# Performance work log

Hardware: AMD Instinct MI355X
Metric: run time of the kernel (lower is better)

## Reference

```python
import jax, jax.numpy as jnp
import numpy as np


def conv2d(x, w, groups=1, pad=0):
    # x: [N,C,H,W], w: [O, C//groups, kh, kw]
    return jax.lax.conv_general_dilated(
        x, w, window_strides=(1, 1), padding=[(pad, pad), (pad, pad)],
        dimension_numbers=("NCHW", "OIHW", "NCHW"), feature_group_count=groups)


def l2norm(x, eps=1e-12):
    # torch F.normalize over last dim: x / max(||x||_2, eps)
    n = jnp.sqrt(jnp.sum(x * x, axis=-1, keepdims=True))
    return x / jnp.maximum(n, eps)


def setup_inputs() -> dict:
    key = jax.random.key(0)
    dim, heads, b, H, W = 48, 8, 2, 256, 256
    ks = jax.random.split(key, 20)
    rn = lambda k, shp, s: (jax.random.normal(k, shp, dtype=jnp.float32) * s)
    return {
        "x1": rn(ks[0], (b, dim, H, W), 1.0),
        "x2": rn(ks[1], (b, dim, H, W), 1.0),
        "t1": jnp.ones((heads, 1, 1), jnp.float32),
        "t2": jnp.ones((heads, 1, 1), jnp.float32),
        "qkv1_w": rn(ks[2], (dim * 3, dim, 1, 1), 0.05),
        "qkv1_dw": rn(ks[3], (dim * 3, 1, 3, 3), 0.05),
        "qkv2_w": rn(ks[4], (dim * 3, dim, 1, 1), 0.05),
        "qkv2_dw": rn(ks[5], (dim * 3, 1, 3, 3), 0.05),
        "mid1_w": rn(ks[6], (dim, dim, 1, 1), 0.05),
        "mid2_w": rn(ks[7], (dim, dim, 1, 1), 0.05),
        "pE_w": rn(ks[8], (dim * 8, dim * 2, 1, 1), 0.05),
        "pE_dw": rn(ks[9], (dim * 8, 1, 3, 3), 0.05),
        "pE1_w": rn(ks[10], (dim * 4, dim, 1, 1), 0.05),
        "pE1_dw": rn(ks[11], (dim * 4, 1, 3, 3), 0.05),
        "pE2_w": rn(ks[12], (dim * 4, dim, 1, 1), 0.05),
        "pE2_dw": rn(ks[13], (dim * 4, 1, 3, 3), 0.05),
        "po1_w": rn(ks[14], (dim * 2, dim * 4, 1, 1), 0.05),
        "po2_w": rn(ks[15], (dim * 2, dim * 4, 1, 1), 0.05),
    }


def reference(x1, x2, t1, t2, qkv1_w, qkv1_dw, qkv2_w, qkv2_dw,
              mid1_w, mid2_w, pE_w, pE_dw, pE1_w, pE1_dw,
              pE2_w, pE2_dw, po1_w, po2_w):
    b, c, h, w = x1.shape
    heads = t1.shape[0]
    ch = c // heads  # channels per head

    def to_heads(t):  # [b, c, h, w] -> [b, heads, ch, h*w]
        return t.reshape(b, heads, ch, h * w)

    qkv1 = conv2d(conv2d(x1, qkv1_w), qkv1_dw, groups=3 * c, pad=1)
    q1, k1, v1 = jnp.split(qkv1, 3, axis=1)
    qkv2 = conv2d(conv2d(x2, qkv2_w), qkv2_dw, groups=3 * c, pad=1)
    q2, k2, v2 = jnp.split(qkv2, 3, axis=1)

    q1, k1, v1 = to_heads(q1), to_heads(k1), to_heads(v1)
    q2, k2, v2 = to_heads(q2), to_heads(k2), to_heads(v2)
    q1, k1 = l2norm(q1), l2norm(k1)
    q2, k2 = l2norm(q2), l2norm(k2)

    # channel cross-attention: [b, heads, ch, ch]
    attn1 = jnp.einsum("bhcn,bhdn->bhcd", q2, k1) * t1
    attn2 = jnp.einsum("bhcn,bhdn->bhcd", q1, k2) * t2
    out1 = jnp.einsum("bhcd,bhdn->bhcn", jax.nn.softmax(attn1, axis=-1), v1)
    out2 = jnp.einsum("bhcd,bhdn->bhcn", jax.nn.softmax(attn2, axis=-1), v2)
    out1 = out1.reshape(b, c, h, w)
    out2 = out2.reshape(b, c, h, w)

    x1 = x1 + conv2d(out1, mid1_w)
    x2 = x2 + conv2d(out2, mid2_w)
    out = jnp.concatenate([x1, x2], axis=1)  # [b, 2c, h, w]

    g = conv2d(conv2d(out, pE_w), pE_dw, groups=8 * c, pad=1)  # [b, 8c, h, w]
    g1, g2 = jnp.split(g, 2, axis=1)
    x1 = jax.nn.gelu(g1, approximate=False) * conv2d(conv2d(x1, pE1_w), pE1_dw, groups=4 * c, pad=1)
    x2 = jax.nn.gelu(g2, approximate=False) * conv2d(conv2d(x2, pE2_w), pE2_dw, groups=4 * c, pad=1)

    return out + conv2d(x1, po1_w) + conv2d(x2, po2_w)
```

## Files before the change

kernel.cpp:

```cpp
#include <hip/hip_runtime.h>
#include <math.h>

#define HW_ 65536

typedef __attribute__((ext_vector_type(8))) short b16x8;
typedef __attribute__((ext_vector_type(4))) short b16x4;
typedef __attribute__((ext_vector_type(4))) float f32x4;

__device__ __forceinline__ unsigned short f2b(float f) {
    union { float f; unsigned u; } v; v.f = f;
    unsigned r = v.u + 0x7fffu + ((v.u >> 16) & 1u);
    return (unsigned short)(r >> 16);
}
__device__ __forceinline__ float b2f(unsigned short h) {
    union { unsigned u; float f; } v; v.u = ((unsigned)h) << 16; return v.f;
}
__device__ __forceinline__ float gelu_f(float x) {
    float t = 0.7978845608f * fmaf(0.044715f * x, x * x, x);
    float e = __expf(2.f * t);
    float th = 1.f - 2.f / (e + 1.f);
    return 0.5f * x * (1.f + th);
}

__device__ __forceinline__ float wave_reduce_sum(float v) {
    #pragma unroll
    for (int off = 32; off; off >>= 1) v += __shfl_down(v, off, 64);
    return v;
}

__device__ __forceinline__ size_t baddr(long px, int CC, int g) {
    return (((size_t)(px >> 4)) * CC + g) * 128 + ((size_t)(px & 15) << 3);
}

__global__ __launch_bounds__(256) void wprep_k(
    const float* __restrict__ q1w, const float* __restrict__ q2w,
    const float* __restrict__ m1w, const float* __restrict__ m2w,
    const float* __restrict__ pEw, const float* __restrict__ p1w,
    const float* __restrict__ p2w, const float* __restrict__ o1w,
    const float* __restrict__ o2w,
    const float* __restrict__ q1dw, const float* __restrict__ q2dw,
    const float* __restrict__ pEdw, const float* __restrict__ p1dw,
    const float* __restrict__ p2dw,
    unsigned short* __restrict__ wt, float* __restrict__ dwt)
{
    const int idx = blockIdx.x * 256 + threadIdx.x;
    if (idx < 135168) {
        const int base[8] = {0,9216,18432,21504,24576,61440,98304,116736};
        int s = 0;
        #pragma unroll
        for (int i = 1; i < 8; i++) if (idx >= base[i]) s = i;
        const int local = idx - base[s];
        float v = 0.f;
        if (s < 4) {
            const int m = local >> 6, k = local & 63;
            const float* src = (s == 0) ? q1w : (s == 1) ? q2w : (s == 2) ? m1w : m2w;
            if (k < 48) v = src[m * 48 + k];
        } else if (s < 6) {
            const int br = s - 4;
            const int m = local / 96, k = local % 96;
            if (m < 192) {
                v = pEw[(size_t)(br * 192 + m) * 96 + k];
            } else {
                const float* p12 = br ? p2w : p1w;
                const int lo = br * 48, m2 = m - 192;
                if (k >= lo && k < lo + 48) v = p12[m2 * 48 + (k - lo)];
            }
        } else {
            const int m = local / 192, k = local % 192;
            v = ((s == 6) ? o1w : o2w)[m * 192 + k];
        }
        wt[idx] = f2b(v);
    } else if (idx < 135168 + 9504) {
        const int d = idx - 135168;
        const int dbase[5] = {0,1296,2592,6048,7776};
        const int Cs[5] = {144,144,384,192,192};
        int s = 0;
        #pragma unroll
        for (int i = 1; i < 5; i++) if (d >= dbase[i]) s = i;
        const int local = d - dbase[s], C = Cs[s];
        const int t = local / C, c = local % C;
        const float* src = (s == 0) ? q1dw : (s == 1) ? q2dw : (s == 2) ? pEdw
                         : (s == 3) ? p1dw : p2dw;
        dwt[d] = src[c * 9 + t];
    }
}

template<int BM, int KC, int NT, int BSRC, int EPI, bool GRIDSWAP>
__global__ __launch_bounds__(256) void gemm_k(
    const unsigned short* __restrict__ B16,
    const float* __restrict__ Bf32, int Cin,
    const unsigned short* __restrict__ W16,
    unsigned short* __restrict__ out16, int CCo, int Coff,
    float* __restrict__ outf, const unsigned short* __restrict__ res)
{
    constexpr int MF = BM / 16;
    const int tid = threadIdx.x;
    const int lane = tid & 63, w = tid >> 6;
    const int lm = lane & 15, lk = lane >> 4;
    const int mb = GRIDSWAP ? blockIdx.x : blockIdx.y;
    const int pxblk = GRIDSWAP ? blockIdx.y : blockIdx.x;
    const int m0 = mb * BM;
    const long wavepx = ((long)pxblk * 4 + w) * (NT * 16);
    const long pxb0 = wavepx >> 4;

    f32x4 acc[NT][MF];
    #pragma unroll
    for (int nt = 0; nt < NT; nt++)
        #pragma unroll
        for (int m = 0; m < MF; m++)
            #pragma unroll
            for (int j = 0; j < 4; j++) acc[nt][m][j] = 0.f;

    #pragma unroll
    for (int kc = 0; kc < KC; kc++) {
        b16x8 a[MF];
        #pragma unroll
        for (int m = 0; m < MF; m++)
            a[m] = *(const b16x8*)&W16[(size_t)(m0 + m * 16 + lm) * (KC * 32) + kc * 32 + lk * 8];
        #pragma unroll
        for (int nt = 0; nt < NT; nt++) {
            b16x8 bb;
            if (BSRC == 0) {
                bb = *(const b16x8*)&B16[((pxb0 + nt) * (KC * 4) + (kc * 4 + lk)) * 128 + lm * 8];
            } else {
                const long px = wavepx + nt * 16 + lm;
                const int p = (int)(px & 65535), bat = (int)(px >> 16);
                #pragma unroll
                for (int j = 0; j < 8; j++) {
                    const int c = kc * 32 + lk * 8 + j;
                    float v = (c < Cin) ? Bf32[((size_t)(bat * Cin + c) << 16) + p] : 0.f;
                    bb[j] = (short)f2b(v);
                }
            }
            #pragma unroll
            for (int m = 0; m < MF; m++)
                acc[nt][m] = __builtin_amdgcn_mfma_f32_16x16x32_bf16(a[m], bb, acc[nt][m], 0, 0, 0);
        }
    }

    #pragma unroll
    for (int nt = 0; nt < NT; nt++) {
        const long px = wavepx + nt * 16 + lm;
        #pragma unroll
        for (int m = 0; m < MF; m++) {
            const int mrow = m * 16 + lk * 4;
            if (EPI == 0) {
                b16x4 o;
                #pragma unroll
                for (int j = 0; j < 4; j++) o[j] = (short)f2b(acc[nt][m][j]);
                const int ch = Coff + m0 + mrow;
                *(b16x4*)&out16[((pxb0 + nt) * CCo + (ch >> 3)) * 128 + lm * 8 + (ch & 7)] = o;
            } else if (EPI == 1) {
                const int p = (int)(px & 65535), bat = (int)(px >> 16);
                b16x4 r4 = *(const b16x4*)&res[((pxb0 + nt) * 12 + (mrow >> 3)) * 128 + lm * 8 + (mrow & 7)];
                #pragma unroll
                for (int j = 0; j < 4; j++)
                    outf[((size_t)(bat * 96 + mrow + j) << 16) + p]
                        = acc[nt][m][j] + b2f((unsigned short)r4[j]);
            } else {
                const int p = (int)(px & 65535), bat = (int)(px >> 16);
                #pragma unroll
                for (int j = 0; j < 4; j++) {
                    const size_t adr = ((size_t)(bat * 96 + mrow + j) << 16) + p;
                    outf[adr] += acc[nt][m][j];
                }
            }
        }
    }
}

__device__ __forceinline__ void dw_acc8(
    float acc[4][8], const unsigned short* __restrict__ T, int CC, int g,
    long px0, int y, int x0, const float* __restrict__ wt, int wstr)
{
    #pragma unroll
    for (int dy = -1; dy <= 1; dy++) {
        const int yy = y + dy;
        if ((unsigned)yy >= 256u) continue;
        float w[3][8];
        #pragma unroll
        for (int t = 0; t < 3; t++) {
            const float* wp = wt + (size_t)((dy + 1) * 3 + t) * wstr;
            const float4 a = *(const float4*)wp;
            const float4 b = *(const float4*)(wp + 4);
            w[t][0] = a.x; w[t][1] = a.y; w[t][2] = a.z; w[t][3] = a.w;
            w[t][4] = b.x; w[t][5] = b.y; w[t][6] = b.z; w[t][7] = b.w;
        }
        #pragma unroll
        for (int c = 0; c < 6; c++) {
            const int xx = x0 - 1 + c;
            b16x8 v;
            if ((unsigned)xx < 256u) {
                v = *(const b16x8*)&T[baddr(px0 + dy * 256 + (c - 1), CC, g)];
            } else {
                #pragma unroll
                for (int k = 0; k < 8; k++) v[k] = 0;
            }
            float f[8];
            #pragma unroll
            for (int k = 0; k < 8; k++) f[k] = b2f((unsigned short)v[k]);
            const int ilo = (c - 2 < 0) ? 0 : c - 2;
            const int ihi = (c < 3) ? c : 3;
            #pragma unroll
            for (int i = ilo; i <= ihi; i++)
                #pragma unroll
                for (int j = 0; j < 8; j++)
                    acc[i][j] = fmaf(w[c - i][j], f[j], acc[i][j]);
        }
    }
}

__global__ __launch_bounds__(256) void dw144_k(
    const unsigned short* __restrict__ in1, unsigned short* __restrict__ out1,
    const unsigned short* __restrict__ in2, unsigned short* __restrict__ out2,
    const float* __restrict__ dwt)
{
    const int z = blockIdx.z;
    const unsigned short* in = z ? in2 : in1;
    unsigned short* out = z ? out2 : out1;
    const float* wt = dwt + z * 1296;
    const int bx = blockIdx.x;
    const int sb = (bx & 7) * 288 + (bx >> 3);
    const int idx = sb * 256 + threadIdx.x;
    const int pb = idx / 72;
    const int rem = idx - pb * 72;
    const int g = rem >> 2, i = rem & 3;
    const long px0 = (long)pb * 16 + i * 4;
    const int y = (int)((px0 & 65535) >> 8), x0 = (int)(px0 & 255);

    float acc[4][8];
    #pragma unroll
    for (int a = 0; a < 4; a++)
        #pragma unroll
        for (int j = 0; j < 8; j++) acc[a][j] = 0.f;
    dw_acc8(acc, in, 18, g, px0, y, x0, wt + g * 8, 144);
    #pragma unroll
    for (int a = 0; a < 4; a++) {
        b16x8 o;
        #pragma unroll
        for (int j = 0; j < 8; j++) o[j] = (short)f2b(acc[a][j]);
        *(b16x8*)&out[baddr(px0 + a, 18, g)] = o;
    }
}

__global__ __launch_bounds__(256) void dwtail_k(
    const unsigned short* __restrict__ GH, unsigned short* __restrict__ Xg,
    const float* __restrict__ dwtG, const float* __restrict__ dwtH)
{
    const int bx = blockIdx.x;
    const int sb = (bx & 7) * 384 + (bx >> 3);
    const int idx = sb * 256 + threadIdx.x;
    const int pb = idx / 96;
    const int rem = idx - pb * 96;
    const int g = rem >> 2, i = rem & 3;
    const long px0 = (long)pb * 16 + i * 4;
    const int y = (int)((px0 & 65535) >> 8), x0 = (int)(px0 & 255);

    float aG[4][8], aH[4][8];
    #pragma unroll
    for (int a = 0; a < 4; a++)
        #pragma unroll
        for (int j = 0; j < 8; j++) { aG[a][j] = 0.f; aH[a][j] = 0.f; }
    dw_acc8(aG, GH, 48, g,      px0, y, x0, dwtG + g * 8, 384);
    dw_acc8(aH, GH, 48, 24 + g, px0, y, x0, dwtH + g * 8, 192);

    #pragma unroll
    for (int a = 0; a < 4; a++) {
        b16x8 o;
        #pragma unroll
        for (int j = 0; j < 8; j++)
            o[j] = (short)f2b(gelu_f(aG[a][j]) * aH[a][j]);
        *(b16x8*)&Xg[baddr(px0 + a, 24, g)] = o;
    }
}

__global__ __launch_bounds__(256) void attnA_k(
    const unsigned short* __restrict__ Q1, const unsigned short* __restrict__ Q2,
    float* __restrict__ part)
{
    const int tid = threadIdx.x;
    const int chunk = blockIdx.x, bh = blockIdx.y, a = blockIdx.z;
    const int b = bh >> 3, h = bh & 7;
    const unsigned* Qq = (const unsigned*)(a ? Q1 : Q2);
    const unsigned* Qk = (const unsigned*)(a ? Q2 : Q1);
    const int u0 = h * 3;
    const int cq = u0 >> 2, o = u0 & 3;
    const int ck = (24 + u0) >> 2;

    float dot[36], nq[6], nk[6];
    #pragma unroll
    for (int i = 0; i < 36; i++) dot[i] = 0.f;
    #pragma unroll
    for (int i = 0; i < 6; i++) { nq[i] = 0.f; nk[i] = 0.f; }

    #pragma unroll 1
    for (int r = 0; r < 8; r++) {
        const long px = (long)b * 65536 + chunk * 2048 + r * 256 + tid;
        const size_t rowu = ((size_t)(px >> 4)) * 18 * 64 + ((px & 15) << 2);
        const uint4 qa = *(const uint4*)&Qq[rowu + (size_t)cq * 64];
        const uint4 qb = *(const uint4*)&Qq[rowu + (size_t)(cq + 1) * 64];
        const uint4 ka = *(const uint4*)&Qk[rowu + (size_t)ck * 64];
        const uint4 kb = *(const uint4*)&Qk[rowu + (size_t)(ck + 1) * 64];
        unsigned uq[3], uk[3];
        if (o == 0)      { uq[0]=qa.x; uq[1]=qa.y; uq[2]=qa.z; uk[0]=ka.x; uk[1]=ka.y; uk[2]=ka.z; }
        else if (o == 1) { uq[0]=qa.y; uq[1]=qa.z; uq[2]=qa.w; uk[0]=ka.y; uk[1]=ka.z; uk[2]=ka.w; }
        else if (o == 2) { uq[0]=qa.z; uq[1]=qa.w; uq[2]=qb.x; uk[0]=ka.z; uk[1]=ka.w; uk[2]=kb.x; }
        else             { uq[0]=qa.w; uq[1]=qb.x; uq[2]=qb.y; uk[0]=ka.w; uk[1]=kb.x; uk[2]=kb.y; }
        float q[6], k[6];
        #pragma unroll
        for (int i = 0; i < 3; i++) {
            union { unsigned u; float f; } lo, hi;
            lo.u = uq[i] << 16; hi.u = uq[i] & 0xFFFF0000u;
            q[2 * i] = lo.f; q[2 * i + 1] = hi.f;
            lo.u = uk[i] << 16; hi.u = uk[i] & 0xFFFF0000u;
            k[2 * i] = lo.f; k[2 * i + 1] = hi.f;
        }
        #pragma unroll
        for (int c = 0; c < 6; c++) nq[c] = fmaf(q[c], q[c], nq[c]);
        #pragma unroll
        for (int d = 0; d < 6; d++) nk[d] = fmaf(k[d], k[d], nk[d]);
        #pragma unroll
        for (int c = 0; c < 6; c++)
            #pragma unroll
            for (int d = 0; d < 6; d++) dot[c * 6 + d] = fmaf(q[c], k[d], dot[c * 6 + d]);
    }

    __shared__ float red[4][48];
    const int lane = tid & 63, wid = tid >> 6;
    #pragma unroll
    for (int i = 0; i < 48; i++) {
        float v = (i < 36) ? dot[i] : (i < 42 ? nq[i - 36] : nk[i - 42]);
        v = wave_reduce_sum(v);
        if (!lane) red[wid][i] = v;
    }
    __syncthreads();
    if (tid < 48)
        part[((size_t)((a * 16 + bh) * 32 + chunk)) * 48 + tid]
            = red[0][tid] + red[1][tid] + red[2][tid] + red[3][tid];
}

__global__ void attnB_k(const float* __restrict__ part,
                        const float* __restrict__ t1, const float* __restrict__ t2,
                        float* __restrict__ att)
{
    const int abh = blockIdx.x, tid = threadIdx.x;
    const int a = abh >> 4, b = (abh >> 3) & 1, h = abh & 7;
    __shared__ float s[48];
    if (tid < 48) {
        float v = 0.f;
        for (int ch = 0; ch < 32; ch++) v += part[((size_t)abh * 32 + ch) * 48 + tid];
        s[tid] = v;
    }
    __syncthreads();
    if (tid < 6) {
        const int c = tid;
        const float tv = a ? t2[h] : t1[h];
        const float qn = fmaxf(sqrtf(s[36 + c]), 1e-12f);
        float raw[6];
        #pragma unroll
        for (int d = 0; d < 6; d++)
            raw[d] = tv * s[c * 6 + d] / (qn * fmaxf(sqrtf(s[42 + d]), 1e-12f));
        float m = raw[0];
        #pragma unroll
        for (int d = 1; d < 6; d++) m = fmaxf(m, raw[d]);
        float e[6], sum = 0.f;
        #pragma unroll
        for (int d = 0; d < 6; d++) { e[d] = expf(raw[d] - m); sum += e[d]; }
        const float inv = 1.f / sum;
        #pragma unroll
        for (int d = 0; d < 6; d++)
            att[((size_t)(a * 2 + b) * 8 + h) * 36 + c * 6 + d] = e[d] * inv;
    }
}

__global__ __launch_bounds__(256) void mid_k(
    const unsigned short* __restrict__ Q1, const unsigned short* __restrict__ Q2,
    const float* __restrict__ att,
    const float* __restrict__ x1, const float* __restrict__ x2,
    const unsigned short* __restrict__ Wm, unsigned short* __restrict__ D16p)
{
    const int br = blockIdx.y;
    const unsigned short* Qv = br ? Q2 : Q1;
    const float* x = br ? x2 : x1;
    const unsigned short* W16 = Wm + br * 3072;
    const float* attb = att + br * 576;
    const int boff = br * 48;

    __shared__ float atts[288];
    __shared__ unsigned short S[256][72];
    const int tid = threadIdx.x;
    const long px = (long)blockIdx.x * 256 + tid;
    const int bat = (int)(px >> 16);

    for (int i = tid; i < 288; i += 256) atts[i] = attb[bat * 288 + i];

    float v[48];
    #pragma unroll
    for (int i = 0; i < 6; i++) {
        b16x8 t = *(const b16x8*)&Qv[baddr(px, 18, 12 + i)];
        #pragma unroll
        for (int j = 0; j < 8; j++) v[i * 8 + j] = b2f((unsigned short)t[j]);
    }
    __syncthreads();

    #pragma unroll
    for (int h = 0; h < 8; h++) {
        unsigned short sh[6];
        #pragma unroll
        for (int c = 0; c < 6; c++) {
            float s = 0.f;
            #pragma unroll
            for (int d = 0; d < 6; d++) s = fmaf(atts[h * 36 + c * 6 + d], v[h * 6 + d], s);
            sh[c] = f2b(s);
        }
        #pragma unroll
        for (int i = 0; i < 3; i++) {
            unsigned packed = (unsigned)sh[2 * i] | ((unsigned)sh[2 * i + 1] << 16);
            *(unsigned*)&S[tid][h * 6 + 2 * i] = packed;
        }
    }
    #pragma unroll
    for (int i = 0; i < 8; i++) *(unsigned*)&S[tid][48 + 2 * i] = 0u;
    __syncthreads();

    const int lane = tid & 63, w = tid >> 6;
    const int lm = lane & 15, lk = lane >> 4;
    f32x4 acc[4][3];
    #pragma unroll
    for (int nt = 0; nt < 4; nt++)
        #pragma unroll
        for (int m = 0; m < 3; m++)
            #pragma unroll
            for (int j = 0; j < 4; j++) acc[nt][m][j] = 0.f;

    #pragma unroll
    for (int kc = 0; kc < 2; kc++) {
        b16x8 a[3];
        #pragma unroll
        for (int m = 0; m < 3; m++)
            a[m] = *(const b16x8*)&W16[(size_t)(m * 16 + lm) * 64 + kc * 32 + lk * 8];
        #pragma unroll
        for (int nt = 0; nt < 4; nt++) {
            b16x8 bb = *(const b16x8*)&S[w * 64 + nt * 16 + lm][kc * 32 + lk * 8];
            #pragma unroll
            for (int m = 0; m < 3; m++)
                acc[nt][m] = __builtin_amdgcn_mfma_f32_16x16x32_bf16(a[m], bb, acc[nt][m], 0, 0, 0);
        }
    }

    #pragma unroll
    for (int nt = 0; nt < 4; nt++) {
        const long px2 = (long)blockIdx.x * 256 + w * 64 + nt * 16 + lm;
        const int p2 = (int)(px2 & 65535);
        const long pxb2 = px2 >> 4;
        #pragma unroll
        for (int m = 0; m < 3; m++) {
            const int row = m * 16 + lk * 4;
            b16x4 o;
            #pragma unroll
            for (int j = 0; j < 4; j++) {
                float xv = x[((size_t)(bat * 48 + row + j) << 16) + p2];
                o[j] = (short)f2b(acc[nt][m][j] + xv);
            }
            const int ch = boff + row;
            *(b16x4*)&D16p[(pxb2 * 12 + (ch >> 3)) * 128 + lm * 8 + (ch & 7)] = o;
        }
    }
}

extern "C" void kernel_launch(void* const* d_in, const int* in_sizes, int n_in,
                              void* d_out, int out_size, void* d_ws, size_t ws_size,
                              hipStream_t stream) {
    const float* x1      = (const float*)d_in[0];
    const float* x2      = (const float*)d_in[1];
    const float* t1      = (const float*)d_in[2];
    const float* t2      = (const float*)d_in[3];
    const float* qkv1_w  = (const float*)d_in[4];
    const float* qkv1_dw = (const float*)d_in[5];
    const float* qkv2_w  = (const float*)d_in[6];
    const float* qkv2_dw = (const float*)d_in[7];
    const float* mid1_w  = (const float*)d_in[8];
    const float* mid2_w  = (const float*)d_in[9];
    const float* pE_w    = (const float*)d_in[10];
    const float* pE_dw   = (const float*)d_in[11];
    const float* pE1_w   = (const float*)d_in[12];
    const float* pE1_dw  = (const float*)d_in[13];
    const float* pE2_w   = (const float*)d_in[14];
    const float* pE2_dw  = (const float*)d_in[15];
    const float* po1_w   = (const float*)d_in[16];
    const float* po2_w   = (const float*)d_in[17];
    float* dout = (float*)d_out;
    char* ws = (char*)d_ws;

    unsigned short* D16p  = (unsigned short*)(ws + 0);
    unsigned short* QKVc1 = (unsigned short*)(ws + 25165824);
    unsigned short* QKVc2 = (unsigned short*)(ws + 62914560);
    unsigned short* Q1    = (unsigned short*)(ws + 100663296);
    unsigned short* Q2    = (unsigned short*)(ws + 138412032);
    unsigned short* GH    = (unsigned short*)(ws + 25165824);
    unsigned short* Xg    = (unsigned short*)(ws + 125829120);
    float*          PART  = (float*)(ws + 176160768);
    float*          ATT   = (float*)(ws + 176357376);
    unsigned short* W16   = (unsigned short*)(ws + 176361984);
    float*          DWT   = (float*)(ws + 176632320);

    const dim3 blk(256);

    wprep_k<<<dim3(566), blk, 0, stream>>>(
        qkv1_w, qkv2_w, mid1_w, mid2_w, pE_w, pE1_w, pE2_w, po1_w, po2_w,
        qkv1_dw, qkv2_dw, pE_dw, pE1_dw, pE2_dw, W16, DWT);

    gemm_k<144,2,4,1,0,false><<<dim3(512,1), blk, 0, stream>>>(
        nullptr, x1, 48, W16, QKVc1, 18, 0, nullptr, nullptr);
    gemm_k<144,2,4,1,0,false><<<dim3(512,1), blk, 0, stream>>>(
        nullptr, x2, 48, W16 + 9216, QKVc2, 18, 0, nullptr, nullptr);
    dw144_k<<<dim3(2304,1,2), blk, 0, stream>>>(QKVc1, Q1, QKVc2, Q2, DWT);

    attnA_k<<<dim3(32,16,2), blk, 0, stream>>>(Q1, Q2, PART);
    attnB_k<<<dim3(32), dim3(64), 0, stream>>>(PART, t1, t2, ATT);

    mid_k<<<dim3(512,2), blk, 0, stream>>>(Q1, Q2, ATT, x1, x2, W16 + 18432, D16p);

    for (int br = 0; br < 2; br++) {
        gemm_k<192,3,2,0,0,true><<<dim3(2,1024), blk, 0, stream>>>(
            D16p, nullptr, 0, W16 + 24576 + br * 36864, GH, 48, 0,
            nullptr, nullptr);
        dwtail_k<<<dim3(3072), blk, 0, stream>>>(
            GH, Xg, DWT + 2592 + br * 192, DWT + (br ? 7776 : 6048));
        if (br == 0)
            gemm_k<96,6,4,0,1,false><<<dim3(512,1), blk, 0, stream>>>(
                Xg, nullptr, 0, W16 + 98304, nullptr, 0, 0, dout, D16p);
        else
            gemm_k<96,6,4,0,2,false><<<dim3(512,1), blk, 0, stream>>>(
                Xg, nullptr, 0, W16 + 116736, nullptr, 0, 0, dout, nullptr);
    }
}
```

Measured before the change: 411.9 us.

## Rewrite depthwise conv row loads with precomputed addresses and retune GEMM tiles

The depthwise 3x3 kernels now compute a base address once and load each row as six 16-byte chunks, using precomputed left/right neighbour offsets instead of calling baddr per tap. bf16 values are unpacked with shifts and masks. The dwtail kernel gets a launch-bounds occupancy hint. Several GEMM launches are retuned to smaller tile counts with twice as many blocks, trading per-block reuse for more parallelism.

```diff
diff --git a/kernel.cpp b/kernel.cpp
--- a/kernel.cpp
+++ b/kernel.cpp
@@ -169,43 +169,50 @@
     }
 }
 
-__device__ __forceinline__ void dw_acc8(
-    float acc[4][8], const unsigned short* __restrict__ T, int CC, int g,
-    long px0, int y, int x0, const float* __restrict__ wt, int wstr)
-{
-    #pragma unroll
-    for (int dy = -1; dy <= 1; dy++) {
-        const int yy = y + dy;
-        if ((unsigned)yy >= 256u) continue;
-        float w[3][8];
-        #pragma unroll
-        for (int t = 0; t < 3; t++) {
-            const float* wp = wt + (size_t)((dy + 1) * 3 + t) * wstr;
-            const float4 a = *(const float4*)wp;
-            const float4 b = *(const float4*)(wp + 4);
-            w[t][0] = a.x; w[t][1] = a.y; w[t][2] = a.z; w[t][3] = a.w;
-            w[t][4] = b.x; w[t][5] = b.y; w[t][6] = b.z; w[t][7] = b.w;
-        }
-        #pragma unroll
-        for (int c = 0; c < 6; c++) {
-            const int xx = x0 - 1 + c;
-            b16x8 v;
-            if ((unsigned)xx < 256u) {
-                v = *(const b16x8*)&T[baddr(px0 + dy * 256 + (c - 1), CC, g)];
-            } else {
-                #pragma unroll
-                for (int k = 0; k < 8; k++) v[k] = 0;
-            }
-            float f[8];
-            #pragma unroll
-            for (int k = 0; k < 8; k++) f[k] = b2f((unsigned short)v[k]);
-            const int ilo = (c - 2 < 0) ? 0 : c - 2;
-            const int ihi = (c < 3) ? c : 3;
-            #pragma unroll
-            for (int i = ilo; i <= ihi; i++)
+__device__ __forceinline__ void unpack8(const uint4 u, float f[8]) {
+    union { unsigned u; float f; } a;
+    a.u = u.x << 16;         f[0] = a.f;
+    a.u = u.x & 0xFFFF0000u; f[1] = a.f;
+    a.u = u.y << 16;         f[2] = a.f;
+    a.u = u.y & 0xFFFF0000u; f[3] = a.f;
+    a.u = u.z << 16;         f[4] = a.f;
+    a.u = u.z & 0xFFFF0000u; f[5] = a.f;
+    a.u = u.w << 16;         f[6] = a.f;
+    a.u = u.w & 0xFFFF0000u; f[7] = a.f;
+}
+
+__device__ __forceinline__ void dw_row4(
+    float acc[4][8], const unsigned short* __restrict__ T,
+    size_t cb, long lOff, long rOff, bool lval, bool rval,
+    const float* __restrict__ wrow, int wstr)
+{
+    float w[3][8];
+    #pragma unroll
+    for (int tx = 0; tx < 3; tx++) {
+        const float4 a = *(const float4*)(wrow + (size_t)tx * wstr);
+        const float4 b = *(const float4*)(wrow + (size_t)tx * wstr + 4);
+        w[tx][0] = a.x; w[tx][1] = a.y; w[tx][2] = a.z; w[tx][3] = a.w;
+        w[tx][4] = b.x; w[tx][5] = b.y; w[tx][6] = b.z; w[tx][7] = b.w;
+    }
+    uint4 u[6];
+    if (lval) u[0] = *(const uint4*)&T[cb + lOff];
+    else      u[0] = make_uint4(0u, 0u, 0u, 0u);
+    #pragma unroll
+    for (int c = 0; c < 4; c++) u[c + 1] = *(const uint4*)&T[cb + (size_t)c * 8];
+    if (rval) u[5] = *(const uint4*)&T[cb + rOff];
+    else      u[5] = make_uint4(0u, 0u, 0u, 0u);
+
+    #pragma unroll
+    for (int d = 0; d < 6; d++) {
+        float f[8];
+        unpack8(u[d], f);
+        #pragma unroll
+        for (int tx = 0; tx < 3; tx++) {
+            const int p = d - tx;
+            if (p >= 0 && p < 4)
                 #pragma unroll
                 for (int j = 0; j < 8; j++)
-                    acc[i][j] = fmaf(w[c - i][j], f[j], acc[i][j]);
+                    acc[p][j] = fmaf(w[tx][j], f[j], acc[p][j]);
         }
     }
 }
@@ -222,55 +229,88 @@
     const int bx = blockIdx.x;
     const int sb = (bx & 7) * 288 + (bx >> 3);
     const int idx = sb * 256 + threadIdx.x;
-    const int pb = idx / 72;
-    const int rem = idx - pb * 72;
+    const int pbi = idx / 72;
+    const int rem = idx - pbi * 72;
     const int g = rem >> 2, i = rem & 3;
-    const long px0 = (long)pb * 16 + i * 4;
-    const int y = (int)((px0 & 65535) >> 8), x0 = (int)(px0 & 255);
+    const long px0 = (long)pbi * 16 + i * 4;
+    const int x0 = (int)(px0 & 255);
+    const int y = (int)((px0 >> 8) & 255);
+    const bool lval = x0 > 0, rval = x0 < 252;
+    const int off = (int)(px0 & 15) * 8;
+    const size_t cb0 = ((size_t)(px0 >> 4) * 18 + g) * 128 + off;
+    const long lOff = (off == 0) ? (120 - 18 * 128) : -8;
+    const long rOff = (off == 96) ? (18 * 128 - 96) : 32;
+    const long dyStep = 16 * 18 * 128;
 
     float acc[4][8];
     #pragma unroll
-    for (int a = 0; a < 4; a++)
-        #pragma unroll
-        for (int j = 0; j < 8; j++) acc[a][j] = 0.f;
-    dw_acc8(acc, in, 18, g, px0, y, x0, wt + g * 8, 144);
-    #pragma unroll
-    for (int a = 0; a < 4; a++) {
+    for (int p = 0; p < 4; p++)
+        #pragma unroll
+        for (int j = 0; j < 8; j++) acc[p][j] = 0.f;
+
+    #pragma unroll
+    for (int dy = -1; dy <= 1; dy++) {
+        const int yy = y + dy;
+        if ((unsigned)yy >= 256u) continue;
+        const size_t cb = cb0 + (size_t)((long)dy * dyStep);
+        dw_row4(acc, in, cb, lOff, rOff, lval, rval,
+                wt + g * 8 + (size_t)(dy + 1) * 3 * 144, 144);
+    }
+
+    #pragma unroll
+    for (int p = 0; p < 4; p++) {
         b16x8 o;
         #pragma unroll
-        for (int j = 0; j < 8; j++) o[j] = (short)f2b(acc[a][j]);
-        *(b16x8*)&out[baddr(px0 + a, 18, g)] = o;
-    }
-}
-
-__global__ __launch_bounds__(256) void dwtail_k(
+        for (int j = 0; j < 8; j++) o[j] = (short)f2b(acc[p][j]);
+        *(b16x8*)&out[cb0 + (size_t)p * 8] = o;
+    }
+}
+
+__global__ __launch_bounds__(256, 4) void dwtail_k(
     const unsigned short* __restrict__ GH, unsigned short* __restrict__ Xg,
     const float* __restrict__ dwtG, const float* __restrict__ dwtH)
 {
     const int bx = blockIdx.x;
     const int sb = (bx & 7) * 384 + (bx >> 3);
     const int idx = sb * 256 + threadIdx.x;
-    const int pb = idx / 96;
-    const int rem = idx - pb * 96;
+    const int pbi = idx / 96;
+    const int rem = idx - pbi * 96;
     const int g = rem >> 2, i = rem & 3;
-    const long px0 = (long)pb * 16 + i * 4;
-    const int y = (int)((px0 & 65535) >> 8), x0 = (int)(px0 & 255);
+    const long px0 = (long)pbi * 16 + i * 4;
+    const int x0 = (int)(px0 & 255);
+    const int y = (int)((px0 >> 8) & 255);
+    const bool lval = x0 > 0, rval = x0 < 252;
+    const int off = (int)(px0 & 15) * 8;
+    const size_t cb0 = ((size_t)(px0 >> 4) * 48 + g) * 128 + off;
+    const long lOff = (off == 0) ? (120 - 48 * 128) : -8;
+    const long rOff = (off == 96) ? (48 * 128 - 96) : 32;
+    const long dyStep = 16 * 48 * 128;
 
     float aG[4][8], aH[4][8];
     #pragma unroll
-    for (int a = 0; a < 4; a++)
-        #pragma unroll
-        for (int j = 0; j < 8; j++) { aG[a][j] = 0.f; aH[a][j] = 0.f; }
-    dw_acc8(aG, GH, 48, g,      px0, y, x0, dwtG + g * 8, 384);
-    dw_acc8(aH, GH, 48, 24 + g, px0, y, x0, dwtH + g * 8, 192);
-
-    #pragma unroll
-    for (int a = 0; a < 4; a++) {
+    for (int p = 0; p < 4; p++)
+        #pragma unroll
+        for (int j = 0; j < 8; j++) { aG[p][j] = 0.f; aH[p][j] = 0.f; }
+
+    #pragma unroll
+    for (int dy = -1; dy <= 1; dy++) {
+        const int yy = y + dy;
+        if ((unsigned)yy >= 256u) continue;
+        const size_t cb = cb0 + (size_t)((long)dy * dyStep);
+        dw_row4(aG, GH, cb, lOff, rOff, lval, rval,
+                dwtG + g * 8 + (size_t)(dy + 1) * 3 * 384, 384);
+        dw_row4(aH, GH, cb + 3072, lOff, rOff, lval, rval,
+                dwtH + g * 8 + (size_t)(dy + 1) * 3 * 192, 192);
+    }
+
+    const size_t ob = ((size_t)(px0 >> 4) * 24 + g) * 128 + off;
+    #pragma unroll
+    for (int p = 0; p < 4; p++) {
         b16x8 o;
         #pragma unroll
         for (int j = 0; j < 8; j++)
-            o[j] = (short)f2b(gelu_f(aG[a][j]) * aH[a][j]);
-        *(b16x8*)&Xg[baddr(px0 + a, 24, g)] = o;
+            o[j] = (short)f2b(gelu_f(aG[p][j]) * aH[p][j]);
+        *(b16x8*)&Xg[ob + (size_t)p * 8] = o;
     }
 }
 
@@ -510,9 +550,9 @@
         qkv1_w, qkv2_w, mid1_w, mid2_w, pE_w, pE1_w, pE2_w, po1_w, po2_w,
         qkv1_dw, qkv2_dw, pE_dw, pE1_dw, pE2_dw, W16, DWT);
 
-    gemm_k<144,2,4,1,0,false><<<dim3(512,1), blk, 0, stream>>>(
+    gemm_k<144,2,2,1,0,false><<<dim3(1024,1), blk, 0, stream>>>(
         nullptr, x1, 48, W16, QKVc1, 18, 0, nullptr, nullptr);
-    gemm_k<144,2,4,1,0,false><<<dim3(512,1), blk, 0, stream>>>(
+    gemm_k<144,2,2,1,0,false><<<dim3(1024,1), blk, 0, stream>>>(
         nullptr, x2, 48, W16 + 9216, QKVc2, 18, 0, nullptr, nullptr);
     dw144_k<<<dim3(2304,1,2), blk, 0, stream>>>(QKVc1, Q1, QKVc2, Q2, DWT);
 
@@ -522,16 +562,16 @@
     mid_k<<<dim3(512,2), blk, 0, stream>>>(Q1, Q2, ATT, x1, x2, W16 + 18432, D16p);
 
     for (int br = 0; br < 2; br++) {
-        gemm_k<192,3,2,0,0,true><<<dim3(2,1024), blk, 0, stream>>>(
+        gemm_k<96,3,2,0,0,true><<<dim3(4,1024), blk, 0, stream>>>(
             D16p, nullptr, 0, W16 + 24576 + br * 36864, GH, 48, 0,
             nullptr, nullptr);
         dwtail_k<<<dim3(3072), blk, 0, stream>>>(
             GH, Xg, DWT + 2592 + br * 192, DWT + (br ? 7776 : 6048));
         if (br == 0)
-            gemm_k<96,6,4,0,1,false><<<dim3(512,1), blk, 0, stream>>>(
+            gemm_k<96,6,2,0,1,false><<<dim3(1024,1), blk, 0, stream>>>(
                 Xg, nullptr, 0, W16 + 98304, nullptr, 0, 0, dout, D16p);
         else
-            gemm_k<96,6,4,0,2,false><<<dim3(512,1), blk, 0, stream>>>(
+            gemm_k<96,6,2,0,2,false><<<dim3(1024,1), blk, 0, stream>>>(
                 Xg, nullptr, 0, W16 + 116736, nullptr, 0, 0, dout, nullptr);
     }
 }
```

Result: slower. 644.6 us, median of 3 (+56.5%).
